# Optimization experiments

Hardware: AMD Instinct MI355X
Metric: run time of the kernel (lower is better)

Reference implementation:

```python
import jax, jax.numpy as jnp
import numpy as np

C = 256          # channels
H = 8            # attn heads
DH = C // H      # head dim
G = 2048         # number of graphs
NPG = 100        # nodes per graph
N = G * NPG      # total nodes
EPS = 1e-5       # batchnorm eps


def setup_inputs() -> dict:
    key = jax.random.key(0)
    ks = jax.random.split(key, 14)
    std = 0.02
    inp = {
        "x0": jax.random.normal(ks[0], (N, C), jnp.float32),
        "x1": jax.random.normal(ks[1], (N, C), jnp.float32),
        "batch": jnp.repeat(jnp.arange(G, dtype=jnp.int64), NPG)[:, None],
        # branch 0: linear + BN affine
        "p0_W": jax.random.normal(ks[2], (C, C), jnp.float32) * std,
        "p0_b": jnp.zeros((C,), jnp.float32),
        "p0_g": jnp.ones((C,), jnp.float32),
        "p0_beta": jnp.zeros((C,), jnp.float32),
        # branch 1
        "p1_W": jax.random.normal(ks[3], (C, C), jnp.float32) * std,
        "p1_b": jnp.zeros((C,), jnp.float32),
        "p1_g": jnp.ones((C,), jnp.float32),
        "p1_beta": jnp.zeros((C,), jnp.float32),
        # merge
        "merge_W": jax.random.normal(ks[4], (C, 2 * C), jnp.float32) * std,
        "merge_b": jnp.zeros((C,), jnp.float32),
        # MHA in_proj (packed q,k,v as in torch) and out_proj
        "in_proj_W": jax.random.normal(ks[5], (3 * C, C), jnp.float32) * std,
        "in_proj_b": jnp.zeros((3 * C,), jnp.float32),
        "out_proj_W": jax.random.normal(ks[6], (C, C), jnp.float32) * std,
        "out_proj_b": jnp.zeros((C,), jnp.float32),
        # readout
        "readout_W": jax.random.normal(ks[7], (1, C), jnp.float32) * std,
        "readout_b": jnp.zeros((1,), jnp.float32),
    }
    return inp


def _lin_bn_relu(x, W, b, g, beta):
    y = x @ W.T + b
    mu = jnp.mean(y, axis=0)
    var = jnp.var(y, axis=0)  # biased, matches torch BN training normalization
    return jax.nn.relu((y - mu) * jax.lax.rsqrt(var + EPS) * g + beta)


def reference(x0, x1, batch,
              p0_W, p0_b, p0_g, p0_beta,
              p1_W, p1_b, p1_g, p1_beta,
              merge_W, merge_b,
              in_proj_W, in_proj_b,
              out_proj_W, out_proj_b,
              readout_W, readout_b):
    seg = batch[:, 0]                                   # [N] sorted graph ids
    h0 = _lin_bn_relu(x0, p0_W, p0_b, p0_g, p0_beta)
    h1 = _lin_bn_relu(x1, p1_W, p1_b, p1_g, p1_beta)
    x = jnp.concatenate([h0, h1], axis=1) @ merge_W.T + merge_b  # [N,C]

    Wq, Wk, Wv = jnp.split(in_proj_W, 3, axis=0)
    bq, bk, bv = jnp.split(in_proj_b, 3, axis=0)
    # query is all-ones (length-1 sequence), shared across graphs
    q = (jnp.ones((C,), x.dtype) @ Wq.T + bq).reshape(H, DH) / jnp.sqrt(jnp.float32(DH))
    k = (x @ Wk.T + bk).reshape(-1, H, DH)              # [N,H,dh]
    v = (x @ Wv.T + bv).reshape(-1, H, DH)              # [N,H,dh]

    scores = jnp.einsum('hd,nhd->nh', q, k)            # [N,H]
    # segmented softmax over nodes of each graph
    m = jax.ops.segment_max(scores, seg, num_segments=G)      # [G,H]
    e = jnp.exp(scores - m[seg])                               # [N,H]
    denom = jax.ops.segment_sum(e, seg, num_segments=G)       # [G,H]
    pooled = jax.ops.segment_sum(e[:, :, None] * v, seg, num_segments=G)  # [G,H,dh]
    pooled = pooled / denom[:, :, None]

    attn = pooled.reshape(G, C) @ out_proj_W.T + out_proj_b   # [G,C]
    out = jnp.tanh(attn @ readout_W.T + readout_b)            # [G,1]
    return out
```

## Files before the change

### kernel.cpp

```cpp
#include <hip/hip_runtime.h>
#include <stdint.h>

#define NROWS 204800
#define NBLK_Y 1600
#define GRP 2048
#define NPG 100

typedef __attribute__((ext_vector_type(4))) float f32x4;
typedef __attribute__((ext_vector_type(8))) short bf16x8;
typedef __attribute__((ext_vector_type(4))) short bf16x4;

__device__ __forceinline__ unsigned bcu(float f){ union{float f;unsigned u;}c; c.f=f; return c.u; }
__device__ __forceinline__ float bcf(unsigned u){ union{unsigned u;float f;}c; c.u=u; return c.f; }
__device__ __forceinline__ short f2bf_rne(float f){ unsigned u=bcu(f); unsigned r=(u+0x7fffu+((u>>16)&1u))>>16; return (short)r; }
__device__ __forceinline__ unsigned pk_trunc(float lo, float hi){
  return __builtin_amdgcn_perm(bcu(hi), bcu(lo), 0x07060302u);
}
__device__ __forceinline__ f32x4 mfma16(bf16x8 a, bf16x8 b, f32x4 c){
  return __builtin_amdgcn_mfma_f32_16x16x32_bf16(a, b, c, 0, 0, 0);
}
#define BFLY16(v) { v += __shfl_xor(v,1); v += __shfl_xor(v,2); v += __shfl_xor(v,4); v += __shfl_xor(v,8); }

__global__ void k_cast_w(const float* __restrict__ w0, const float* __restrict__ w1,
                         short* __restrict__ out){
  int t = blockIdx.x*256 + threadIdx.x;
  const float* src = (t < 16384) ? w0 : w1;
  int base = (t & 16383) * 4;
  f32x4 v = *(const f32x4*)(src + base);
  bf16x4 o; o[0]=f2bf_rne(v[0]); o[1]=f2bf_rne(v[1]); o[2]=f2bf_rne(v[2]); o[3]=f2bf_rne(v[3]);
  *(bf16x4*)(out + ((t<16384)?0:65536) + base) = o;
}

__global__ __attribute__((amdgpu_waves_per_eu(2, 2))) void __launch_bounds__(256)
k_gemm_y(const float* __restrict__ x0, const float* __restrict__ x1,
         const short* __restrict__ Wb,
         const float* __restrict__ b0p, const float* __restrict__ b1p,
         short* __restrict__ y0, short* __restrict__ y1,
         float* __restrict__ stats){
  __shared__ float st_sh[4][256][2];
  int bid = blockIdx.x;
  int which = (bid >= NBLK_Y) ? 1 : 0;
  const float* __restrict__ X = which ? x1 : x0;
  short* __restrict__ Y = which ? y1 : y0;
  const short* __restrict__ W = Wb + which*65536;
  const float* __restrict__ bias = which ? b1p : b0p;
  int n0 = (which ? bid - NBLK_Y : bid) * 128;
  int t = threadIdx.x, lane = t & 63, w = t >> 6;
  int l15 = lane & 15, q = lane >> 4;
  int nb = n0 + w*32;

  const short* wrow = W + l15*256;

  bf16x8 wfA[4], wfB[4];
  #pragma unroll
  for (int ks=0; ks<4; ks++)
    wfA[ks] = *(const bf16x8*)(wrow + ks*32 + q*8);

  bf16x8 xb[2][8];
  #pragma unroll
  for (int g=0; g<2; g++){
    const float* xr = X + (nb + g*16 + l15)*256;
    #pragma unroll
    for (int ks=0; ks<8; ks++){
      int kq = ks*32 + q*8;
      f32x4 a = *(const f32x4*)(xr + kq);
      f32x4 b = *(const f32x4*)(xr + kq + 4);
      int4 p; p.x=(int)pk_trunc(a[0],a[1]); p.y=(int)pk_trunc(a[2],a[3]);
              p.z=(int)pk_trunc(b[0],b[1]); p.w=(int)pk_trunc(b[2],b[3]);
      xb[g][ks] = __builtin_bit_cast(bf16x8, p);
    }
  }

  short* yo0 = Y + (nb + l15)*256 + q*4;
  short* yo1 = Y + (nb + 16 + l15)*256 + q*4;

  #pragma unroll
  for (int mt=0; mt<16; mt++){
    #pragma unroll
    for (int ks=0; ks<4; ks++)
      wfB[ks] = *(const bf16x8*)(wrow + mt*4096 + (ks+4)*32 + q*8);
    f32x4 acc0 = f32x4{0,0,0,0}, acc1 = f32x4{0,0,0,0};
    #pragma unroll
    for (int ks=0; ks<4; ks++){
      acc0 = mfma16(wfA[ks], xb[0][ks], acc0);
      acc1 = mfma16(wfA[ks], xb[1][ks], acc1);
    }
    if (mt < 15){
      #pragma unroll
      for (int ks=0; ks<4; ks++)
        wfA[ks] = *(const bf16x8*)(wrow + (mt+1)*4096 + ks*32 + q*8);
    }
    #pragma unroll
    for (int ks=0; ks<4; ks++){
      acc0 = mfma16(wfB[ks], xb[0][ks+4], acc0);
      acc1 = mfma16(wfB[ks], xb[1][ks+4], acc1);
    }
    f32x4 bb = *(const f32x4*)(bias + mt*16 + q*4);
    f32x4 v0 = acc0 + bb;
    f32x4 v1 = acc1 + bb;
    int2 s0v; s0v.x=(int)pk_trunc(v0[0],v0[1]); s0v.y=(int)pk_trunc(v0[2],v0[3]);
    *(int2*)(yo0 + mt*16) = s0v;
    int2 s1v; s1v.x=(int)pk_trunc(v1[0],v1[1]); s1v.y=(int)pk_trunc(v1[2],v1[3]);
    *(int2*)(yo1 + mt*16) = s1v;
    float sa0=v0[0]+v1[0], sa1=v0[1]+v1[1], sa2=v0[2]+v1[2], sa3=v0[3]+v1[3];
    float qa0=v0[0]*v0[0]+v1[0]*v1[0], qa1=v0[1]*v0[1]+v1[1]*v1[1];
    float qa2=v0[2]*v0[2]+v1[2]*v1[2], qa3=v0[3]*v0[3]+v1[3]*v1[3];
    BFLY16(sa0); BFLY16(sa1); BFLY16(sa2); BFLY16(sa3);
    BFLY16(qa0); BFLY16(qa1); BFLY16(qa2); BFLY16(qa3);
    if (l15 == 0){
      int c0 = mt*16 + q*4;
      st_sh[w][c0+0][0]=sa0; st_sh[w][c0+0][1]=qa0;
      st_sh[w][c0+1][0]=sa1; st_sh[w][c0+1][1]=qa1;
      st_sh[w][c0+2][0]=sa2; st_sh[w][c0+2][1]=qa2;
      st_sh[w][c0+3][0]=sa3; st_sh[w][c0+3][1]=qa3;
    }
  }
  __syncthreads();
  {
    float ss = st_sh[0][t][0]+st_sh[1][t][0]+st_sh[2][t][0]+st_sh[3][t][0];
    float qq = st_sh[0][t][1]+st_sh[1][t][1]+st_sh[2][t][1]+st_sh[3][t][1];
    int rep = bid & 7;
    atomicAdd(&stats[rep*1024 + which*512 + t], ss);
    atomicAdd(&stats[rep*1024 + which*512 + 256 + t], qq);
  }
}

__global__ void k_small(const float* __restrict__ inW, const float* __restrict__ inB,
                        const float* __restrict__ mergeB,
                        const float* __restrict__ g0, const float* __restrict__ be0,
                        const float* __restrict__ g1, const float* __restrict__ be1,
                        const float* __restrict__ outW, const float* __restrict__ outB,
                        const float* __restrict__ rout, const float* __restrict__ routB,
                        const float* __restrict__ stats,
                        float* __restrict__ prm, float* __restrict__ qk){
  __shared__ float qv_sh[256], ck_sh[256];
  int t = threadIdx.x;
  const float invN = 1.0f/(float)NROWS;
  float s0=0, sq0=0, s1=0, sq1=0;
  for (int r=0;r<8;r++){
    s0  += stats[r*1024 + t];       sq0 += stats[r*1024 + 256 + t];
    s1  += stats[r*1024 + 512 + t]; sq1 += stats[r*1024 + 768 + t];
  }
  {
    float mu = s0*invN, var = sq0*invN - mu*mu;
    float rs = rsqrtf(var + 1e-5f);
    float a = g0[t]*rs;
    prm[t] = a; prm[512+t] = be0[t] - mu*a;
  }
  {
    float mu = s1*invN, var = sq1*invN - mu*mu;
    float rs = rsqrtf(var + 1e-5f);
    float a = g1[t]*rs;
    prm[256+t] = a; prm[768+t] = be1[t] - mu*a;
  }
  float qs = inB[t];
  for (int k=0;k<256;k++) qs += inW[t*256 + k];
  qv_sh[t] = qs * 0.17677669529663689f;
  float cks = inB[256+t];
  for (int m=0;m<256;m++) cks += mergeB[m] * inW[(256+t)*256 + m];
  ck_sh[t] = cks;
  float cvs = inB[512+t];
  for (int m=0;m<256;m++) cvs += mergeB[m] * inW[(512+t)*256 + m];
  prm[1024+t] = cvs;
  float wf = 0;
  for (int m=0;m<256;m++) wf += rout[m] * outW[m*256 + t];
  prm[1288+t] = wf;
  __syncthreads();
  for (int r=0;r<8;r++){
    int idx = r*256 + t; int h = idx>>8, m = idx&255;
    float s = 0;
    for (int d=0;d<32;d++) s += qv_sh[h*32+d] * inW[(256 + h*32 + d)*256 + m];
    qk[h*256+m] = s;
  }
  if (t < 8){
    float cs_ = 0;
    for (int d=0;d<32;d++) cs_ += qv_sh[t*32+d]*ck_sh[t*32+d];
    prm[1280+t] = cs_;
  }
  if (t == 0){
    float cf = routB[0];
    for (int m=0;m<256;m++) cf += rout[m]*outB[m];
    prm[1544] = cf;
  }
}

__global__ void k_wall(const float* __restrict__ inW, const float* __restrict__ mergeW,
                       const float* __restrict__ qk, short* __restrict__ Wall){
  int c = blockIdx.x; int t = threadIdx.x;
  if (c >= 264){
    Wall[c*512 + t] = 0; Wall[c*512 + 256 + t] = 0; return;
  }
  const float* src = (c < 256) ? (inW + (512+c)*256) : (qk + (c-256)*256);
  float a0=0, a1=0;
  for (int m=0;m<256;m++){
    float wm = src[m];
    a0 += wm * mergeW[m*512 + t];
    a1 += wm * mergeW[m*512 + 256 + t];
  }
  Wall[c*512 + t]       = f2bf_rne(a0);
  Wall[c*512 + 256 + t] = f2bf_rne(a1);
}

__global__ __attribute__((amdgpu_waves_per_eu(2, 2))) void __launch_bounds__(256)
k_fused(const short* __restrict__ y0, const short* __restrict__ y1,
        const short* __restrict__ Wall, const float* __restrict__ prm,
        float* __restrict__ num, float* __restrict__ den){
  __shared__ float a_sh[512], b_sh[512], cv_sh[256], cs_sh[8];
  int t = threadIdx.x, lane = t & 63, w = t >> 6;
  int l15 = lane & 15, q = lane >> 4;
  for (int i=t; i<512; i+=256){ a_sh[i] = prm[i]; b_sh[i] = prm[512+i]; }
  cv_sh[t] = prm[1024+t];
  if (t < 8) cs_sh[t] = prm[1280+t];
  __syncthreads();

  int n0 = blockIdx.x*128, nb = n0 + w*32;
  const short* wbase = Wall + l15*512;

  bf16x8 wfA[8], wfB[8];
  #pragma unroll
  for (int ks=0; ks<8; ks++)
    wfA[ks] = *(const bf16x8*)(wbase + 16*8192 + ks*32 + q*8);

  bf16x8 xb[2][16];
  #pragma unroll
  for (int ks=0; ks<16; ks++){
    int jq = ks*32 + q*8;
    const short* ybase = (ks < 8) ? y0 : y1;
    int jj = jq & 255;
    f32x4 paL = *(const f32x4*)&a_sh[jq];  f32x4 paH = *(const f32x4*)&a_sh[jq+4];
    f32x4 pbL = *(const f32x4*)&b_sh[jq];  f32x4 pbH = *(const f32x4*)&b_sh[jq+4];
    #pragma unroll
    for (int g=0; g<2; g++){
      int4 raw = *(const int4*)(ybase + (nb + g*16 + l15)*256 + jj);
      unsigned r0=(unsigned)raw.x, r1=(unsigned)raw.y, r2=(unsigned)raw.z, r3=(unsigned)raw.w;
      float h0 = fmaxf(fmaf(bcf(r0<<16),         paL[0], pbL[0]), 0.f);
      float h1 = fmaxf(fmaf(bcf(r0&0xffff0000u), paL[1], pbL[1]), 0.f);
      float h2 = fmaxf(fmaf(bcf(r1<<16),         paL[2], pbL[2]), 0.f);
      float h3 = fmaxf(fmaf(bcf(r1&0xffff0000u), paL[3], pbL[3]), 0.f);
      float h4 = fmaxf(fmaf(bcf(r2<<16),         paH[0], pbH[0]), 0.f);
      float h5 = fmaxf(fmaf(bcf(r2&0xffff0000u), paH[1], pbH[1]), 0.f);
      float h6 = fmaxf(fmaf(bcf(r3<<16),         paH[2], pbH[2]), 0.f);
      float h7 = fmaxf(fmaf(bcf(r3&0xffff0000u), paH[3], pbH[3]), 0.f);
      int4 pk; pk.x=(int)pk_trunc(h0,h1); pk.y=(int)pk_trunc(h2,h3);
               pk.z=(int)pk_trunc(h4,h5); pk.w=(int)pk_trunc(h6,h7);
      xb[g][ks] = __builtin_bit_cast(bf16x8, pk);
    }
  }

  float e0[4], e1[4];

  #pragma unroll
  for (int idx=0; idx<17; idx++){
    const int T = (idx==0) ? 16 : (idx-1);
    #pragma unroll
    for (int ks=0; ks<8; ks++)
      wfB[ks] = *(const bf16x8*)(wbase + T*8192 + (ks+8)*32 + q*8);
    f32x4 acc0 = f32x4{0,0,0,0}, acc1 = f32x4{0,0,0,0};
    #pragma unroll
    for (int ks=0; ks<8; ks++){
      acc0 = mfma16(wfA[ks], xb[0][ks], acc0);
      acc1 = mfma16(wfA[ks], xb[1][ks], acc1);
    }
    if (idx < 16){
      #pragma unroll
      for (int ks=0; ks<8; ks++)
        wfA[ks] = *(const bf16x8*)(wbase + idx*8192 + ks*32 + q*8);
    }
    #pragma unroll
    for (int ks=0; ks<8; ks++){
      acc0 = mfma16(wfB[ks], xb[0][ks+8], acc0);
      acc1 = mfma16(wfB[ks], xb[1][ks+8], acc1);
    }

    if (T == 16){
      #pragma unroll
      for (int i=0;i<4;i++){
        float cadd = (q<2) ? cs_sh[q*4+i] : 0.f;
        e0[i] = (q<2) ? __expf(acc0[i] + cadd) : 0.f;
        e1[i] = (q<2) ? __expf(acc1[i] + cadd) : 0.f;
      }
      #pragma unroll
      for (int nt=0; nt<2; nt++){
        int tb = nb + nt*16;
        int sg = tb/100; int brow = (sg+1)*100 - tb; bool split = brow < 16;
        float d0[4], d1[4];
        #pragma unroll
        for (int i=0;i<4;i++){
          float ev = nt ? e1[i] : e0[i];
          d0[i] = (l15 < brow) ? ev : 0.f; d1[i] = ev - d0[i];
        }
        BFLY16(d0[0]); BFLY16(d0[1]); BFLY16(d0[2]); BFLY16(d0[3]);
        if (split){ BFLY16(d1[0]); BFLY16(d1[1]); BFLY16(d1[2]); BFLY16(d1[3]); }
        if (l15==0 && q<2){
          #pragma unroll
          for (int i=0;i<4;i++) atomicAdd(&den[sg*8 + q*4 + i], d0[i]);
          if (split){
            #pragma unroll
            for (int i=0;i<4;i++) atomicAdd(&den[(sg+1)*8 + q*4 + i], d1[i]);
          }
        }
      }
    } else {
      const int h = T>>1, hq = h>>2, hi = h&3;
      f32x4 cvv = *(const f32x4*)&cv_sh[T*16 + q*4];
      #pragma unroll
      for (int nt=0; nt<2; nt++){
        float esrc = nt ? e1[hi] : e0[hi];
        float eb = __shfl(esrc, hq*16 + l15, 64);
        int tb = nb + nt*16;
        int sg = tb/100; int brow = (sg+1)*100 - tb; bool split = brow < 16;
        f32x4 accg = nt ? acc1 : acc0;
        float p0[4], p1[4];
        #pragma unroll
        for (int i=0;i<4;i++){
          float wv = (accg[i] + cvv[i]) * eb;
          p0[i] = (l15 < brow) ? wv : 0.f; p1[i] = wv - p0[i];
        }
        BFLY16(p0[0]); BFLY16(p0[1]); BFLY16(p0[2]); BFLY16(p0[3]);
        if (split){ BFLY16(p1[0]); BFLY16(p1[1]); BFLY16(p1[2]); BFLY16(p1[3]); }
        if (l15==0){
          int c0 = T*16 + q*4;
          #pragma unroll
          for (int i=0;i<4;i++) atomicAdd(&num[sg*256 + c0 + i], p0[i]);
          if (split){
            #pragma unroll
            for (int i=0;i<4;i++) atomicAdd(&num[(sg+1)*256 + c0 + i], p1[i]);
          }
        }
      }
    }
  }
}

__global__ void k_out(const float* __restrict__ num, const float* __restrict__ den,
                      const float* __restrict__ prm, float* __restrict__ out){
  int g = blockIdx.x; int lane = threadIdx.x;
  f32x4 nm = *(const f32x4*)(num + g*256 + lane*4);
  f32x4 wf = *(const f32x4*)(prm + 1288 + lane*4);
  float dh = den[g*8 + (lane>>3)];
  float v = (nm[0]*wf[0] + nm[1]*wf[1] + nm[2]*wf[2] + nm[3]*wf[3]) / dh;
  v += __shfl_xor(v,1); v += __shfl_xor(v,2); v += __shfl_xor(v,4);
  v += __shfl_xor(v,8); v += __shfl_xor(v,16); v += __shfl_xor(v,32);
  if (lane==0) out[g] = tanhf(v + prm[1544]);
}

extern "C" void kernel_launch(void* const* d_in, const int* in_sizes, int n_in,
                              void* d_out, int out_size, void* d_ws, size_t ws_size,
                              hipStream_t stream){
  const float* x0      = (const float*)d_in[0];
  const float* x1      = (const float*)d_in[1];
  const float* p0_W    = (const float*)d_in[3];
  const float* p0_b    = (const float*)d_in[4];
  const float* p0_g    = (const float*)d_in[5];
  const float* p0_beta = (const float*)d_in[6];
  const float* p1_W    = (const float*)d_in[7];
  const float* p1_b    = (const float*)d_in[8];
  const float* p1_g    = (const float*)d_in[9];
  const float* p1_beta = (const float*)d_in[10];
  const float* merge_W = (const float*)d_in[11];
  const float* merge_b = (const float*)d_in[12];
  const float* inp_W   = (const float*)d_in[13];
  const float* inp_b   = (const float*)d_in[14];
  const float* out_W   = (const float*)d_in[15];
  const float* out_b   = (const float*)d_in[16];
  const float* ro_W    = (const float*)d_in[17];
  const float* ro_b    = (const float*)d_in[18];
  float* outp = (float*)d_out;

  char* ws = (char*)d_ws;
  short* y0w   = (short*)(ws);
  short* y1w   = (short*)(ws + 104857600);
  short* Wb    = (short*)(ws + 209715200);
  short* Wall  = (short*)(ws + 209977344);
  float* stats = (float*)(ws + 210255872);
  float* num   = (float*)(ws + 210288640);
  float* den   = (float*)(ws + 212385792);
  float* prm   = (float*)(ws + 212451328);
  float* qk    = (float*)(ws + 212459520);

  hipMemsetAsync(ws + 210255872, 0, 2195456, stream);

  k_cast_w<<<dim3(128), dim3(256), 0, stream>>>(p0_W, p1_W, Wb);
  k_gemm_y<<<dim3(2*NBLK_Y), dim3(256), 0, stream>>>(x0, x1, Wb, p0_b, p1_b, y0w, y1w, stats);
  k_small<<<dim3(1), dim3(256), 0, stream>>>(inp_W, inp_b, merge_b, p0_g, p0_beta, p1_g, p1_beta,
                                             out_W, out_b, ro_W, ro_b, stats, prm, qk);
  k_wall<<<dim3(272), dim3(256), 0, stream>>>(inp_W, merge_W, qk, Wall);
  k_fused<<<dim3(NBLK_Y), dim3(256), 0, stream>>>(y0w, y1w, Wall, prm, num, den);
  k_out<<<dim3(GRP), dim3(64), 0, stream>>>(num, den, prm, outp);
}
```

Before: 985.3 us.

## Stage activations through swizzled LDS with coalesced loads; halve fused-kernel rows per block

Both GEMM kernels now load activation rows cooperatively with coalesced row-wise loads into XOR-swizzled shared memory, then read MFMA fragments from LDS each iteration instead of keeping them all in registers from strided per-lane global loads. The fused kernel processes 64 rows per block (3200 blocks) with one 16-row tile per wave and reads BN/prm parameters directly from global memory. The aim is better global coalescing and lower register pressure. The cost is extra LDS traffic and a barrier, and the smaller tiles reload the weights more often.

```diff
diff --git a/kernel.cpp b/kernel.cpp
--- a/kernel.cpp
+++ b/kernel.cpp
@@ -3,6 +3,7 @@
 
 #define NROWS 204800
 #define NBLK_Y 1600
+#define NBLK_F 3200
 #define GRP 2048
 #define NPG 100
 
@@ -37,6 +38,7 @@
          const float* __restrict__ b0p, const float* __restrict__ b1p,
          short* __restrict__ y0, short* __restrict__ y1,
          float* __restrict__ stats){
+  __shared__ __align__(16) short xs[32768];
   __shared__ float st_sh[4][256][2];
   int bid = blockIdx.x;
   int which = (bid >= NBLK_Y) ? 1 : 0;
@@ -47,43 +49,48 @@
   int n0 = (which ? bid - NBLK_Y : bid) * 128;
   int t = threadIdx.x, lane = t & 63, w = t >> 6;
   int l15 = lane & 15, q = lane >> 4;
-  int nb = n0 + w*32;
+
+  #pragma unroll
+  for (int s=0; s<32; s++){
+    int row = s*4 + w;
+    f32x4 v = *(const f32x4*)(X + (n0+row)*256 + (lane<<2));
+    int2 pk2; pk2.x=(int)pk_trunc(v[0],v[1]); pk2.y=(int)pk_trunc(v[2],v[3]);
+    int byte = (row<<9) + (lane<<3);
+    *(int2*)((char*)xs + (byte ^ ((row&7)<<4))) = pk2;
+  }
 
   const short* wrow = W + l15*256;
-
   bf16x8 wfA[4], wfB[4];
   #pragma unroll
   for (int ks=0; ks<4; ks++)
     wfA[ks] = *(const bf16x8*)(wrow + ks*32 + q*8);
 
-  bf16x8 xb[2][8];
-  #pragma unroll
-  for (int g=0; g<2; g++){
-    const float* xr = X + (nb + g*16 + l15)*256;
-    #pragma unroll
-    for (int ks=0; ks<8; ks++){
-      int kq = ks*32 + q*8;
-      f32x4 a = *(const f32x4*)(xr + kq);
-      f32x4 b = *(const f32x4*)(xr + kq + 4);
-      int4 p; p.x=(int)pk_trunc(a[0],a[1]); p.y=(int)pk_trunc(a[2],a[3]);
-              p.z=(int)pk_trunc(b[0],b[1]); p.w=(int)pk_trunc(b[2],b[3]);
-      xb[g][ks] = __builtin_bit_cast(bf16x8, p);
-    }
-  }
-
-  short* yo0 = Y + (nb + l15)*256 + q*4;
-  short* yo1 = Y + (nb + 16 + l15)*256 + q*4;
+  int pA = (w*32 + l15)*512 + q*16;
+  int pB = pA + 16*512;
+  const int swzC = (l15 & 7) << 4;
+
+  short* yo0 = Y + (n0 + w*32 + l15)*256 + q*4;
+  short* yo1 = yo0 + 16*256;
+
+  __syncthreads();
 
   #pragma unroll
   for (int mt=0; mt<16; mt++){
     #pragma unroll
     for (int ks=0; ks<4; ks++)
       wfB[ks] = *(const bf16x8*)(wrow + mt*4096 + (ks+4)*32 + q*8);
+    asm volatile("" : "+v"(pA), "+v"(pB));
+    bf16x8 xg0[8], xg1[8];
+    #pragma unroll
+    for (int ks=0; ks<8; ks++){
+      xg0[ks] = *(const bf16x8*)((const char*)xs + ((pA + ks*64) ^ swzC));
+      xg1[ks] = *(const bf16x8*)((const char*)xs + ((pB + ks*64) ^ swzC));
+    }
     f32x4 acc0 = f32x4{0,0,0,0}, acc1 = f32x4{0,0,0,0};
     #pragma unroll
     for (int ks=0; ks<4; ks++){
-      acc0 = mfma16(wfA[ks], xb[0][ks], acc0);
-      acc1 = mfma16(wfA[ks], xb[1][ks], acc1);
+      acc0 = mfma16(wfA[ks], xg0[ks], acc0);
+      acc1 = mfma16(wfA[ks], xg1[ks], acc1);
     }
     if (mt < 15){
       #pragma unroll
@@ -92,8 +99,8 @@
     }
     #pragma unroll
     for (int ks=0; ks<4; ks++){
-      acc0 = mfma16(wfB[ks], xb[0][ks+4], acc0);
-      acc1 = mfma16(wfB[ks], xb[1][ks+4], acc1);
+      acc0 = mfma16(wfB[ks], xg0[ks+4], acc0);
+      acc1 = mfma16(wfB[ks], xg1[ks+4], acc1);
     }
     f32x4 bb = *(const f32x4*)(bias + mt*16 + q*4);
     f32x4 v0 = acc0 + bb;
@@ -205,49 +212,50 @@
 k_fused(const short* __restrict__ y0, const short* __restrict__ y1,
         const short* __restrict__ Wall, const float* __restrict__ prm,
         float* __restrict__ num, float* __restrict__ den){
-  __shared__ float a_sh[512], b_sh[512], cv_sh[256], cs_sh[8];
+  __shared__ __align__(16) short xs[32768];
   int t = threadIdx.x, lane = t & 63, w = t >> 6;
   int l15 = lane & 15, q = lane >> 4;
-  for (int i=t; i<512; i+=256){ a_sh[i] = prm[i]; b_sh[i] = prm[512+i]; }
-  cv_sh[t] = prm[1024+t];
-  if (t < 8) cs_sh[t] = prm[1280+t];
-  __syncthreads();
-
-  int n0 = blockIdx.x*128, nb = n0 + w*32;
+  int n0 = blockIdx.x * 64;
+
+  int j0 = (lane & 31)*8 + ((lane >> 5) << 8);
+  f32x4 paL = *(const f32x4*)(prm + j0);
+  f32x4 paH = *(const f32x4*)(prm + j0 + 4);
+  f32x4 pbL = *(const f32x4*)(prm + 512 + j0);
+  f32x4 pbH = *(const f32x4*)(prm + 512 + j0 + 4);
+  f32x4 csv = *(const f32x4*)(prm + 1280 + q*4);
+
   const short* wbase = Wall + l15*512;
-
   bf16x8 wfA[8], wfB[8];
   #pragma unroll
   for (int ks=0; ks<8; ks++)
     wfA[ks] = *(const bf16x8*)(wbase + 16*8192 + ks*32 + q*8);
 
-  bf16x8 xb[2][16];
-  #pragma unroll
-  for (int ks=0; ks<16; ks++){
-    int jq = ks*32 + q*8;
-    const short* ybase = (ks < 8) ? y0 : y1;
-    int jj = jq & 255;
-    f32x4 paL = *(const f32x4*)&a_sh[jq];  f32x4 paH = *(const f32x4*)&a_sh[jq+4];
-    f32x4 pbL = *(const f32x4*)&b_sh[jq];  f32x4 pbH = *(const f32x4*)&b_sh[jq+4];
-    #pragma unroll
-    for (int g=0; g<2; g++){
-      int4 raw = *(const int4*)(ybase + (nb + g*16 + l15)*256 + jj);
-      unsigned r0=(unsigned)raw.x, r1=(unsigned)raw.y, r2=(unsigned)raw.z, r3=(unsigned)raw.w;
-      float h0 = fmaxf(fmaf(bcf(r0<<16),         paL[0], pbL[0]), 0.f);
-      float h1 = fmaxf(fmaf(bcf(r0&0xffff0000u), paL[1], pbL[1]), 0.f);
-      float h2 = fmaxf(fmaf(bcf(r1<<16),         paL[2], pbL[2]), 0.f);
-      float h3 = fmaxf(fmaf(bcf(r1&0xffff0000u), paL[3], pbL[3]), 0.f);
-      float h4 = fmaxf(fmaf(bcf(r2<<16),         paH[0], pbH[0]), 0.f);
-      float h5 = fmaxf(fmaf(bcf(r2&0xffff0000u), paH[1], pbH[1]), 0.f);
-      float h6 = fmaxf(fmaf(bcf(r3<<16),         paH[2], pbH[2]), 0.f);
-      float h7 = fmaxf(fmaf(bcf(r3&0xffff0000u), paH[3], pbH[3]), 0.f);
-      int4 pk; pk.x=(int)pk_trunc(h0,h1); pk.y=(int)pk_trunc(h2,h3);
-               pk.z=(int)pk_trunc(h4,h5); pk.w=(int)pk_trunc(h6,h7);
-      xb[g][ks] = __builtin_bit_cast(bf16x8, pk);
-    }
-  }
-
-  float e0[4], e1[4];
+  const short* ysrc = (lane < 32) ? y0 : y1;
+  #pragma unroll
+  for (int s=0; s<16; s++){
+    int row = s*4 + w;
+    int4 raw = *(const int4*)(ysrc + (n0+row)*256 + (lane&31)*8);
+    unsigned r0=(unsigned)raw.x, r1=(unsigned)raw.y, r2=(unsigned)raw.z, r3=(unsigned)raw.w;
+    float h0 = fmaxf(fmaf(bcf(r0<<16),         paL[0], pbL[0]), 0.f);
+    float h1 = fmaxf(fmaf(bcf(r0&0xffff0000u), paL[1], pbL[1]), 0.f);
+    float h2 = fmaxf(fmaf(bcf(r1<<16),         paL[2], pbL[2]), 0.f);
+    float h3 = fmaxf(fmaf(bcf(r1&0xffff0000u), paL[3], pbL[3]), 0.f);
+    float h4 = fmaxf(fmaf(bcf(r2<<16),         paH[0], pbH[0]), 0.f);
+    float h5 = fmaxf(fmaf(bcf(r2&0xffff0000u), paH[1], pbH[1]), 0.f);
+    float h6 = fmaxf(fmaf(bcf(r3<<16),         paH[2], pbH[2]), 0.f);
+    float h7 = fmaxf(fmaf(bcf(r3&0xffff0000u), paH[3], pbH[3]), 0.f);
+    int4 pk4; pk4.x=(int)pk_trunc(h0,h1); pk4.y=(int)pk_trunc(h2,h3);
+              pk4.z=(int)pk_trunc(h4,h5); pk4.w=(int)pk_trunc(h6,h7);
+    int byte = (row<<10) + ((lane&31)<<4) + ((lane>>5)<<9);
+    *(int4*)((char*)xs + (byte ^ ((row&7)<<4))) = pk4;
+  }
+  __syncthreads();
+
+  int pA = (w*16 + l15)*1024 + q*16;
+  const int swzC = (l15 & 7) << 4;
+  int tb = n0 + w*16;
+  int sg = tb/100; int brow = (sg+1)*100 - tb; bool split = brow < 16;
+  float e0[4];
 
   #pragma unroll
   for (int idx=0; idx<17; idx++){
@@ -255,77 +263,59 @@
     #pragma unroll
     for (int ks=0; ks<8; ks++)
       wfB[ks] = *(const bf16x8*)(wbase + T*8192 + (ks+8)*32 + q*8);
-    f32x4 acc0 = f32x4{0,0,0,0}, acc1 = f32x4{0,0,0,0};
-    #pragma unroll
-    for (int ks=0; ks<8; ks++){
-      acc0 = mfma16(wfA[ks], xb[0][ks], acc0);
-      acc1 = mfma16(wfA[ks], xb[1][ks], acc1);
-    }
+    asm volatile("" : "+v"(pA));
+    bf16x8 xg[16];
+    #pragma unroll
+    for (int ks=0; ks<16; ks++)
+      xg[ks] = *(const bf16x8*)((const char*)xs + ((pA + ks*64) ^ swzC));
+    f32x4 accA = f32x4{0,0,0,0}, accB = f32x4{0,0,0,0};
+    #pragma unroll
+    for (int ks=0; ks<8; ks++) accA = mfma16(wfA[ks], xg[ks], accA);
     if (idx < 16){
       #pragma unroll
       for (int ks=0; ks<8; ks++)
         wfA[ks] = *(const bf16x8*)(wbase + idx*8192 + ks*32 + q*8);
     }
     #pragma unroll
-    for (int ks=0; ks<8; ks++){
-      acc0 = mfma16(wfB[ks], xb[0][ks+8], acc0);
-      acc1 = mfma16(wfB[ks], xb[1][ks+8], acc1);
-    }
+    for (int ks=0; ks<8; ks++) accB = mfma16(wfB[ks], xg[ks+8], accB);
+    f32x4 acc = accA + accB;
 
     if (T == 16){
       #pragma unroll
-      for (int i=0;i<4;i++){
-        float cadd = (q<2) ? cs_sh[q*4+i] : 0.f;
-        e0[i] = (q<2) ? __expf(acc0[i] + cadd) : 0.f;
-        e1[i] = (q<2) ? __expf(acc1[i] + cadd) : 0.f;
-      }
-      #pragma unroll
-      for (int nt=0; nt<2; nt++){
-        int tb = nb + nt*16;
-        int sg = tb/100; int brow = (sg+1)*100 - tb; bool split = brow < 16;
-        float d0[4], d1[4];
+      for (int i=0;i<4;i++)
+        e0[i] = (q<2) ? __expf(acc[i] + csv[i]) : 0.f;
+      float d0[4], d1[4];
+      #pragma unroll
+      for (int i=0;i<4;i++){ d0[i] = (l15 < brow) ? e0[i] : 0.f; d1[i] = e0[i] - d0[i]; }
+      BFLY16(d0[0]); BFLY16(d0[1]); BFLY16(d0[2]); BFLY16(d0[3]);
+      if (split){ BFLY16(d1[0]); BFLY16(d1[1]); BFLY16(d1[2]); BFLY16(d1[3]); }
+      if (l15==0 && q<2){
         #pragma unroll
-        for (int i=0;i<4;i++){
-          float ev = nt ? e1[i] : e0[i];
-          d0[i] = (l15 < brow) ? ev : 0.f; d1[i] = ev - d0[i];
-        }
-        BFLY16(d0[0]); BFLY16(d0[1]); BFLY16(d0[2]); BFLY16(d0[3]);
-        if (split){ BFLY16(d1[0]); BFLY16(d1[1]); BFLY16(d1[2]); BFLY16(d1[3]); }
-        if (l15==0 && q<2){
+        for (int i=0;i<4;i++) atomicAdd(&den[sg*8 + q*4 + i], d0[i]);
+        if (split){
           #pragma unroll
-          for (int i=0;i<4;i++) atomicAdd(&den[sg*8 + q*4 + i], d0[i]);
-          if (split){
-            #pragma unroll
-            for (int i=0;i<4;i++) atomicAdd(&den[(sg+1)*8 + q*4 + i], d1[i]);
-          }
+          for (int i=0;i<4;i++) atomicAdd(&den[(sg+1)*8 + q*4 + i], d1[i]);
         }
       }
     } else {
       const int h = T>>1, hq = h>>2, hi = h&3;
-      f32x4 cvv = *(const f32x4*)&cv_sh[T*16 + q*4];
-      #pragma unroll
-      for (int nt=0; nt<2; nt++){
-        float esrc = nt ? e1[hi] : e0[hi];
-        float eb = __shfl(esrc, hq*16 + l15, 64);
-        int tb = nb + nt*16;
-        int sg = tb/100; int brow = (sg+1)*100 - tb; bool split = brow < 16;
-        f32x4 accg = nt ? acc1 : acc0;
-        float p0[4], p1[4];
+      f32x4 cvv = *(const f32x4*)(prm + 1024 + T*16 + q*4);
+      float eb = __shfl(e0[hi], hq*16 + l15, 64);
+      float pv0[4], pv1[4];
+      #pragma unroll
+      for (int i=0;i<4;i++){
+        float wv = (acc[i] + cvv[i]) * eb;
+        pv0[i] = (l15 < brow) ? wv : 0.f; pv1[i] = wv - pv0[i];
+      }
+      BFLY16(pv0[0]); BFLY16(pv0[1]); BFLY16(pv0[2]); BFLY16(pv0[3]);
+      if (split){ BFLY16(pv1[0]); BFLY16(pv1[1]); BFLY16(pv1[2]); BFLY16(pv1[3]); }
+      if (l15==0){
+        int c0 = T*16 + q*4;
         #pragma unroll
-        for (int i=0;i<4;i++){
-          float wv = (accg[i] + cvv[i]) * eb;
-          p0[i] = (l15 < brow) ? wv : 0.f; p1[i] = wv - p0[i];
-        }
-        BFLY16(p0[0]); BFLY16(p0[1]); BFLY16(p0[2]); BFLY16(p0[3]);
-        if (split){ BFLY16(p1[0]); BFLY16(p1[1]); BFLY16(p1[2]); BFLY16(p1[3]); }
-        if (l15==0){
-          int c0 = T*16 + q*4;
+        for (int i=0;i<4;i++) atomicAdd(&num[sg*256 + c0 + i], pv0[i]);
+        if (split){
           #pragma unroll
-          for (int i=0;i<4;i++) atomicAdd(&num[sg*256 + c0 + i], p0[i]);
-          if (split){
-            #pragma unroll
-            for (int i=0;i<4;i++) atomicAdd(&num[(sg+1)*256 + c0 + i], p1[i]);
-          }
+          for (int i=0;i<4;i++) atomicAdd(&num[(sg+1)*256 + c0 + i], pv1[i]);
         }
       }
     }
@@ -385,6 +375,6 @@
   k_small<<<dim3(1), dim3(256), 0, stream>>>(inp_W, inp_b, merge_b, p0_g, p0_beta, p1_g, p1_beta,
                                              out_W, out_b, ro_W, ro_b, stats, prm, qk);
   k_wall<<<dim3(272), dim3(256), 0, stream>>>(inp_W, merge_W, qk, Wall);
-  k_fused<<<dim3(NBLK_Y), dim3(256), 0, stream>>>(y0w, y1w, Wall, prm, num, den);
+  k_fused<<<dim3(NBLK_F), dim3(256), 0, stream>>>(y0w, y1w, Wall, prm, num, den);
   k_out<<<dim3(GRP), dim3(64), 0, stream>>>(num, den, prm, outp);
 }
```

Result: slower. 1.099 ms (+11.5%).
